# Kernel tuning notes

Hardware: AMD Instinct MI355X
Metric: run time of the kernel (lower is better)

Reference implementation:

```python
import jax, jax.numpy as jnp
import numpy as np

EMIN = 1e-9
EMAX = 1.0
PENAL = 3.0
VOLFRAC = 0.4
GAMMA2 = 1.0
NME = 262144        # number of finite elements
KE = 64             # 8x8 element stiffness entries per element
NDOF = 524288       # global degrees of freedom


def setup_inputs() -> dict:
    key = jax.random.key(0)
    k1, k2, k3, k4, k5 = jax.random.split(key, 5)
    W_x = jax.random.normal(k1, (NME,), dtype=jnp.float32)
    K_sep = jax.random.normal(k2, (NME, KE), dtype=jnp.float32)
    indeces_K = jax.random.randint(k3, (2, NME * KE), 0, NDOF, dtype=jnp.int32)
    u = jax.random.normal(k4, (NDOF,), dtype=jnp.float32)
    f = jax.random.normal(k5, (NDOF,), dtype=jnp.float32)
    return {"W_x": W_x, "K_sep": K_sep, "indeces_K": indeces_K, "u": u, "f": f}


def reference(W_x, K_sep, indeces_K, u, f):
    # SIMP density from logits
    rho = jax.nn.sigmoid(W_x)                                  # [nme]
    # power-law material interpolation: Emin + rho^p (Emax - Emin)
    scale = EMIN + rho ** PENAL * (EMAX - EMIN)                # [nme]
    # scaled element stiffness values, flattened COO values
    sK = (K_sep * scale[:, None]).reshape(-1)                  # [nme*64]
    rows = indeces_K[0]
    cols = indeces_K[1]
    # sparse matvec K @ u via gather + segment-sum scatter assembly
    Ku = jax.ops.segment_sum(sK * u[cols], rows, num_segments=NDOF)  # [ndof]
    confidence_loss = jnp.linalg.norm(Ku - f)
    vofrac_loss = jax.nn.relu(rho.mean() - VOLFRAC)
    loss = vofrac_loss + GAMMA2 * confidence_loss
    return loss
```

## Files before the change

kernel.cpp:

```cpp
#include <hip/hip_runtime.h>
#include <math.h>

namespace {

constexpr int       kNME    = 262144;
constexpr int       kNDOF   = 524288;
constexpr long long kNNZ    = 16777216;
constexpr int       kNB     = 64;
constexpr int       kBShift = 13;
constexpr int       kBSpan  = 8192;
constexpr int       kEnt    = 2048;
constexpr int       kPerTh  = 8;
constexpr int       kCtrStride = 16;

constexpr float kEmin    = 1e-9f;
constexpr float kEmax    = 1.0f;
constexpr float kVolfrac = 0.4f;

using u32   = unsigned;
using i32x4 = __attribute__((ext_vector_type(4))) int;
using f32x4 = __attribute__((ext_vector_type(4))) float;
using u32x4 = __attribute__((ext_vector_type(4))) unsigned;

__device__ __forceinline__ u32 pack32(unsigned localrow, float v) {
    return (localrow << 19) | (__float_as_uint(v) >> 13);
}

__global__ void scale_kernel(const float* __restrict__ W_x,
                             float* __restrict__ scale,
                             float* __restrict__ rho_sum) {
    int i = blockIdx.x * blockDim.x + threadIdx.x;
    float rho = 0.0f;
    if (i < kNME) {
        float x = W_x[i];
        rho = 1.0f / (1.0f + __expf(-x));
        scale[i] = kEmin + rho * rho * rho * (kEmax - kEmin);
    }
    for (int off = 32; off > 0; off >>= 1) rho += __shfl_down(rho, off, 64);
    __shared__ float partial[4];
    const int lane = threadIdx.x & 63;
    const int wid  = threadIdx.x >> 6;
    if (lane == 0) partial[wid] = rho;
    __syncthreads();
    if (threadIdx.x == 0)
        atomicAdd(rho_sum, partial[0] + partial[1] + partial[2] + partial[3]);
}

__global__ __launch_bounds__(256, 8)
void producer_kernel(const float* __restrict__ K_sep,
                     const int*   __restrict__ rows,
                     const int*   __restrict__ cols,
                     const float* __restrict__ u,
                     const float* __restrict__ scale,
                     u32*         __restrict__ pairs,
                     unsigned*    __restrict__ counters,
                     long long chunk_base, unsigned capSub, int R) {
    __shared__ unsigned hist[kNB], ofs[kNB], gbase[kNB];
    __shared__ u32      sorted[kEnt];

    const int tid = threadIdx.x;
    const int sub = blockIdx.x & (R - 1);
    if (tid < kNB) hist[tid] = 0u;
    __syncthreads();

    const long long i0 =
        chunk_base + (long long)blockIdx.x * kEnt + (long long)tid * kPerTh;
    i32x4 r0 = __builtin_nontemporal_load((const i32x4*)(rows + i0));
    i32x4 r1 = __builtin_nontemporal_load((const i32x4*)(rows + i0) + 1);
    i32x4 c0 = __builtin_nontemporal_load((const i32x4*)(cols + i0));
    i32x4 c1 = __builtin_nontemporal_load((const i32x4*)(cols + i0) + 1);
    f32x4 k0 = __builtin_nontemporal_load((const f32x4*)(K_sep + i0));
    f32x4 k1 = __builtin_nontemporal_load((const f32x4*)(K_sep + i0) + 1);
    const float s = scale[(int)(i0 >> 6)];

    unsigned rv[kPerTh];
    float    vv[kPerTh];
#pragma unroll
    for (int j = 0; j < 4; ++j) {
        rv[j]     = (unsigned)r0[j];  vv[j]     = k0[j] * s * u[c0[j]];
        rv[j + 4] = (unsigned)r1[j];  vv[j + 4] = k1[j] * s * u[c1[j]];
    }
#pragma unroll
    for (int j = 0; j < kPerTh; ++j)
        rv[j] |= atomicAdd(&hist[rv[j] >> kBShift], 1u) << 19;
    __syncthreads();

    if (tid < kNB) {
        unsigned h = hist[tid];
        unsigned x = h;
#pragma unroll
        for (int off = 1; off < kNB; off <<= 1) {
            unsigned y = __shfl_up(x, off, 64);
            if (tid >= off) x += y;
        }
        ofs[tid]   = x - h;
        gbase[tid] = atomicAdd(&counters[(tid * R + sub) * kCtrStride], h);
    }
    __syncthreads();

#pragma unroll
    for (int j = 0; j < kPerTh; ++j) {
        unsigned row = rv[j] & 0x7FFFFu;
        unsigned b   = row >> kBShift;
        unsigned pos = ofs[b] + (rv[j] >> 19);
        sorted[pos]  = pack32(row & (kBSpan - 1), vv[j]);
    }
    __syncthreads();

    const int wid = tid >> 6, lane = tid & 63;
    for (int b = wid; b < kNB; b += 4) {
        const unsigned s0 = ofs[b];
        const unsigned n  = hist[b];
        const unsigned g  = gbase[b];
        u32* dst = pairs + (size_t)(b * R + sub) * capSub + g;
        for (unsigned i = lane; i < n; i += 64) {
            if (g + i < capSub)
                __builtin_nontemporal_store(sorted[s0 + i], &dst[i]);
        }
    }
}

__global__ __launch_bounds__(512, 8)
void consumer_kernel(const u32*      __restrict__ pairs,
                     const unsigned* __restrict__ counters,
                     float*          __restrict__ partial,
                     unsigned capSub, int R, int accum) {
    const int b   = blockIdx.x / R;
    const int sub = blockIdx.x - b * R;
    unsigned cnt = counters[(b * R + sub) * kCtrStride];
    if (cnt > capSub) cnt = capSub;

    __shared__ float acc[kBSpan];
    for (int i = threadIdx.x; i < kBSpan; i += 512) acc[i] = 0.0f;
    __syncthreads();

    const u32* p = pairs + (size_t)(b * R + sub) * capSub;
    const unsigned aligned = cnt & ~3u;
    for (unsigned i = 4 * threadIdx.x; i < aligned; i += 4 * 512) {
        u32x4 e = __builtin_nontemporal_load((const u32x4*)(p + i));
#pragma unroll
        for (int j = 0; j < 4; ++j)
            atomicAdd(&acc[e[j] >> 19], __uint_as_float(e[j] << 13));
    }
    if (threadIdx.x < (cnt - aligned)) {
        u32 e = p[aligned + threadIdx.x];
        atomicAdd(&acc[e >> 19], __uint_as_float(e << 13));
    }
    __syncthreads();

    float* dst = partial + (size_t)(b * R + sub) * kBSpan;
    if (accum) {
        for (int i = threadIdx.x; i < kBSpan; i += 512) dst[i] += acc[i];
    } else {
        for (int i = threadIdx.x; i < kBSpan; i += 512) dst[i] = acc[i];
    }
}

__global__ void norm_kernel(const float* __restrict__ partial,
                            const float* __restrict__ f,
                            float* __restrict__ norm_sum, int R) {
    const int b     = blockIdx.x >> 3;
    const int i0    = (blockIdx.x & 7) * 1024 + threadIdx.x * 4;
    f32x4 s = {0.0f, 0.0f, 0.0f, 0.0f};
    for (int r = 0; r < R; ++r)
        s += *(const f32x4*)(partial + (size_t)(b * R + r) * kBSpan + i0);
    f32x4 fv = *(const f32x4*)(f + (size_t)b * kBSpan + i0);
    f32x4 d  = s - fv;
    float a = d[0] * d[0] + d[1] * d[1] + d[2] * d[2] + d[3] * d[3];
    for (int off = 32; off > 0; off >>= 1) a += __shfl_down(a, off, 64);
    __shared__ float partial_s[4];
    const int lane = threadIdx.x & 63;
    const int wid  = threadIdx.x >> 6;
    if (lane == 0) partial_s[wid] = a;
    __syncthreads();
    if (threadIdx.x == 0)
        atomicAdd(norm_sum,
                  partial_s[0] + partial_s[1] + partial_s[2] + partial_s[3]);
}

__global__ void scatter_dev_kernel(const float* __restrict__ K_sep,
                                   const int*   __restrict__ rows,
                                   const int*   __restrict__ cols,
                                   const float* __restrict__ u,
                                   const float* __restrict__ scale,
                                   float* __restrict__ Ku) {
    long long i = (long long)blockIdx.x * blockDim.x + threadIdx.x;
    if (i >= kNNZ) return;
    float s = scale[(int)(i >> 6)];
    atomicAdd(&Ku[rows[i]], K_sep[i] * s * u[cols[i]]);
}

__global__ void norm1_kernel(const float* __restrict__ Ku,
                             const float* __restrict__ f,
                             float* __restrict__ norm_sum) {
    float a = 0.0f;
    for (int i = blockIdx.x * blockDim.x + threadIdx.x; i < kNDOF;
         i += gridDim.x * blockDim.x) {
        float d = Ku[i] - f[i];
        a += d * d;
    }
    for (int off = 32; off > 0; off >>= 1) a += __shfl_down(a, off, 64);
    __shared__ float partial_s[4];
    const int lane = threadIdx.x & 63;
    const int wid  = threadIdx.x >> 6;
    if (lane == 0) partial_s[wid] = a;
    __syncthreads();
    if (threadIdx.x == 0)
        atomicAdd(norm_sum,
                  partial_s[0] + partial_s[1] + partial_s[2] + partial_s[3]);
}

__global__ void finalize_kernel(const float* __restrict__ acc,
                                float* __restrict__ out) {
    if (threadIdx.x == 0 && blockIdx.x == 0) {
        float rho_mean = acc[0] * (1.0f / (float)kNME);
        float vol = fmaxf(rho_mean - kVolfrac, 0.0f);
        out[0] = vol + sqrtf(acc[1]);
    }
}

}

extern "C" void kernel_launch(void* const* d_in, const int* in_sizes, int n_in,
                              void* d_out, int out_size, void* d_ws, size_t ws_size,
                              hipStream_t stream) {
    const float* W_x   = (const float*)d_in[0];
    const float* K_sep = (const float*)d_in[1];
    const int*   idx   = (const int*)d_in[2];
    const float* u     = (const float*)d_in[3];
    const float* f     = (const float*)d_in[4];
    const int* rows = idx;
    const int* cols = idx + kNNZ;

    float* ws = (float*)d_ws;
    const size_t avail = ws_size / sizeof(float);

    struct Opt { int nc, R; unsigned margin; };
    const Opt opts[] = {{1, 16, 2048}, {1, 16, 1024}, {1, 8, 2048},
                        {2, 8, 2048},  {2, 8, 1024},  {4, 8, 1024},
                        {4, 4, 1024},  {8, 4, 1024}};
    int NC = -1, R = 16;
    unsigned capSub = 0;
    size_t ctrF = 0, partialF = 0;
    for (const Opt& o : opts) {
        long long perCell = kNNZ / ((long long)o.nc * kNB * o.R);
        unsigned  mc      = (unsigned)perCell + o.margin;
        size_t cf = (size_t)o.nc * kNB * o.R * kCtrStride;
        size_t pf = (size_t)kNB * o.R * kBSpan;
        size_t need = 16 + cf + pf + (size_t)kNME +
                      (size_t)kNB * o.R * (size_t)mc;
        if (need <= avail) {
            NC = o.nc; R = o.R; capSub = mc; ctrF = cf; partialF = pf;
            break;
        }
    }

    if (NC < 0) {
        float* Ku    = ws;
        float* scale = ws + kNDOF;
        float* acc   = ws + kNDOF + kNME;
        hipMemsetAsync(ws, 0, (size_t)(kNDOF + kNME + 16) * sizeof(float), stream);
        scale_kernel<<<kNME / 256, 256, 0, stream>>>(W_x, scale, acc);
        scatter_dev_kernel<<<(int)(kNNZ / 256), 256, 0, stream>>>(
            K_sep, rows, cols, u, scale, Ku);
        norm1_kernel<<<2048, 256, 0, stream>>>(Ku, f, acc + 1);
        finalize_kernel<<<1, 64, 0, stream>>>(acc, (float*)d_out);
        return;
    }

    float*    acc      = ws;
    unsigned* counters = (unsigned*)(ws + 16);
    float*    partial  = ws + 16 + ctrF;
    float*    scale    = partial + partialF;
    u32*      pairs    = (u32*)(scale + kNME);

    hipMemsetAsync(ws, 0, (16 + ctrF) * sizeof(float), stream);

    scale_kernel<<<kNME / 256, 256, 0, stream>>>(W_x, scale, acc);

    const long long chunk = kNNZ / NC;
    const int prod_blocks = (int)(chunk / kEnt);
    for (int c = 0; c < NC; ++c) {
        unsigned* ctr = counters + (size_t)c * kNB * R * kCtrStride;
        producer_kernel<<<prod_blocks, 256, 0, stream>>>(
            K_sep, rows, cols, u, scale, pairs, ctr, chunk * c, capSub, R);
        consumer_kernel<<<kNB * R, 512, 0, stream>>>(
            pairs, ctr, partial, capSub, R, c > 0 ? 1 : 0);
    }

    norm_kernel<<<kNB * (kBSpan / 1024), 256, 0, stream>>>(
        partial, f, acc + 1, R);

    finalize_kernel<<<1, 64, 0, stream>>>(acc, (float*)d_out);
}
```

Measured before the change: 258.9 us.

## Double producer work per block and vectorize padded bucket writes

```diff
diff --git a/kernel.cpp b/kernel.cpp
--- a/kernel.cpp
+++ b/kernel.cpp
@@ -9,8 +9,9 @@
 constexpr int       kNB     = 64;
 constexpr int       kBShift = 13;
 constexpr int       kBSpan  = 8192;
-constexpr int       kEnt    = 2048;
-constexpr int       kPerTh  = 8;
+constexpr int       kEnt    = 4096;
+constexpr int       kPerTh  = 16;
+constexpr int       kSortN  = kEnt + kNB * 4;
 constexpr int       kCtrStride = 16;
 
 constexpr float kEmin    = 1e-9f;
@@ -46,7 +47,7 @@
         atomicAdd(rho_sum, partial[0] + partial[1] + partial[2] + partial[3]);
 }
 
-__global__ __launch_bounds__(256, 8)
+__global__ __launch_bounds__(256, 6)
 void producer_kernel(const float* __restrict__ K_sep,
                      const int*   __restrict__ rows,
                      const int*   __restrict__ cols,
@@ -55,46 +56,69 @@
                      u32*         __restrict__ pairs,
                      unsigned*    __restrict__ counters,
                      long long chunk_base, unsigned capSub, int R) {
-    __shared__ unsigned hist[kNB], ofs[kNB], gbase[kNB];
-    __shared__ u32      sorted[kEnt];
+    __shared__ unsigned hist[kNB], ofs[kNB], gbase[kNB], h4s[kNB];
+    __shared__ __align__(16) u32 sorted[kSortN];
 
     const int tid = threadIdx.x;
     const int sub = blockIdx.x & (R - 1);
     if (tid < kNB) hist[tid] = 0u;
+    for (int i = tid; i < kSortN / 4; i += 256)
+        ((u32x4*)sorted)[i] = u32x4{0u, 0u, 0u, 0u};
     __syncthreads();
 
     const long long i0 =
         chunk_base + (long long)blockIdx.x * kEnt + (long long)tid * kPerTh;
-    i32x4 r0 = __builtin_nontemporal_load((const i32x4*)(rows + i0));
-    i32x4 r1 = __builtin_nontemporal_load((const i32x4*)(rows + i0) + 1);
-    i32x4 c0 = __builtin_nontemporal_load((const i32x4*)(cols + i0));
-    i32x4 c1 = __builtin_nontemporal_load((const i32x4*)(cols + i0) + 1);
-    f32x4 k0 = __builtin_nontemporal_load((const f32x4*)(K_sep + i0));
-    f32x4 k1 = __builtin_nontemporal_load((const f32x4*)(K_sep + i0) + 1);
     const float s = scale[(int)(i0 >> 6)];
 
     unsigned rv[kPerTh];
     float    vv[kPerTh];
-#pragma unroll
-    for (int j = 0; j < 4; ++j) {
-        rv[j]     = (unsigned)r0[j];  vv[j]     = k0[j] * s * u[c0[j]];
-        rv[j + 4] = (unsigned)r1[j];  vv[j + 4] = k1[j] * s * u[c1[j]];
-    }
-#pragma unroll
-    for (int j = 0; j < kPerTh; ++j)
-        rv[j] |= atomicAdd(&hist[rv[j] >> kBShift], 1u) << 19;
+    {
+        i32x4 r0 = __builtin_nontemporal_load((const i32x4*)(rows + i0));
+        i32x4 r1 = __builtin_nontemporal_load((const i32x4*)(rows + i0) + 1);
+        i32x4 c0 = __builtin_nontemporal_load((const i32x4*)(cols + i0));
+        i32x4 c1 = __builtin_nontemporal_load((const i32x4*)(cols + i0) + 1);
+        f32x4 k0 = __builtin_nontemporal_load((const f32x4*)(K_sep + i0));
+        f32x4 k1 = __builtin_nontemporal_load((const f32x4*)(K_sep + i0) + 1);
+#pragma unroll
+        for (int j = 0; j < 4; ++j) {
+            rv[j]     = (unsigned)r0[j];  vv[j]     = k0[j] * s * u[c0[j]];
+            rv[j + 4] = (unsigned)r1[j];  vv[j + 4] = k1[j] * s * u[c1[j]];
+        }
+#pragma unroll
+        for (int j = 0; j < 8; ++j)
+            rv[j] |= atomicAdd(&hist[rv[j] >> kBShift], 1u) << 19;
+    }
+    {
+        const long long i8 = i0 + 8;
+        i32x4 r0 = __builtin_nontemporal_load((const i32x4*)(rows + i8));
+        i32x4 r1 = __builtin_nontemporal_load((const i32x4*)(rows + i8) + 1);
+        i32x4 c0 = __builtin_nontemporal_load((const i32x4*)(cols + i8));
+        i32x4 c1 = __builtin_nontemporal_load((const i32x4*)(cols + i8) + 1);
+        f32x4 k0 = __builtin_nontemporal_load((const f32x4*)(K_sep + i8));
+        f32x4 k1 = __builtin_nontemporal_load((const f32x4*)(K_sep + i8) + 1);
+#pragma unroll
+        for (int j = 0; j < 4; ++j) {
+            rv[8 + j]  = (unsigned)r0[j];  vv[8 + j]  = k0[j] * s * u[c0[j]];
+            rv[12 + j] = (unsigned)r1[j];  vv[12 + j] = k1[j] * s * u[c1[j]];
+        }
+#pragma unroll
+        for (int j = 8; j < 16; ++j)
+            rv[j] |= atomicAdd(&hist[rv[j] >> kBShift], 1u) << 19;
+    }
     __syncthreads();
 
     if (tid < kNB) {
-        unsigned h = hist[tid];
-        unsigned x = h;
+        unsigned h  = hist[tid];
+        unsigned h4 = (h + 3u) & ~3u;
+        unsigned x  = h4;
 #pragma unroll
         for (int off = 1; off < kNB; off <<= 1) {
             unsigned y = __shfl_up(x, off, 64);
             if (tid >= off) x += y;
         }
-        ofs[tid]   = x - h;
-        gbase[tid] = atomicAdd(&counters[(tid * R + sub) * kCtrStride], h);
+        ofs[tid]   = x - h4;
+        h4s[tid]   = h4;
+        gbase[tid] = atomicAdd(&counters[(tid * R + sub) * kCtrStride], h4);
     }
     __syncthreads();
 
@@ -110,12 +134,14 @@
     const int wid = tid >> 6, lane = tid & 63;
     for (int b = wid; b < kNB; b += 4) {
         const unsigned s0 = ofs[b];
-        const unsigned n  = hist[b];
+        const unsigned n4 = h4s[b];
         const unsigned g  = gbase[b];
+        if (g >= capSub) continue;
+        const unsigned m = min(n4, capSub - g);
         u32* dst = pairs + (size_t)(b * R + sub) * capSub + g;
-        for (unsigned i = lane; i < n; i += 64) {
-            if (g + i < capSub)
-                __builtin_nontemporal_store(sorted[s0 + i], &dst[i]);
+        for (unsigned i = lane * 4; i < m; i += 256) {
+            u32x4 w = *(const u32x4*)&sorted[s0 + i];
+            __builtin_nontemporal_store(w, (u32x4*)(dst + i));
         }
     }
 }
@@ -159,8 +185,8 @@
 __global__ void norm_kernel(const float* __restrict__ partial,
                             const float* __restrict__ f,
                             float* __restrict__ norm_sum, int R) {
-    const int b     = blockIdx.x >> 3;
-    const int i0    = (blockIdx.x & 7) * 1024 + threadIdx.x * 4;
+    const int b  = blockIdx.x >> 3;
+    const int i0 = (blockIdx.x & 7) * 1024 + threadIdx.x * 4;
     f32x4 s = {0.0f, 0.0f, 0.0f, 0.0f};
     for (int r = 0; r < R; ++r)
         s += *(const f32x4*)(partial + (size_t)(b * R + r) * kBSpan + i0);
```

New measurement: 281.0 us. 8.5% more time.

## Fuse scale and finalize into producer/norm, pad buckets for vector stores

Applied to the files above, without the earlier changes.

```diff
diff --git a/kernel.cpp b/kernel.cpp
--- a/kernel.cpp
+++ b/kernel.cpp
@@ -11,6 +11,7 @@
 constexpr int       kBSpan  = 8192;
 constexpr int       kEnt    = 2048;
 constexpr int       kPerTh  = 8;
+constexpr int       kSortN  = kEnt + kNB * 4;
 constexpr int       kCtrStride = 16;
 
 constexpr float kEmin    = 1e-9f;
@@ -24,26 +25,6 @@
 
 __device__ __forceinline__ u32 pack32(unsigned localrow, float v) {
     return (localrow << 19) | (__float_as_uint(v) >> 13);
-}
-
-__global__ void scale_kernel(const float* __restrict__ W_x,
-                             float* __restrict__ scale,
-                             float* __restrict__ rho_sum) {
-    int i = blockIdx.x * blockDim.x + threadIdx.x;
-    float rho = 0.0f;
-    if (i < kNME) {
-        float x = W_x[i];
-        rho = 1.0f / (1.0f + __expf(-x));
-        scale[i] = kEmin + rho * rho * rho * (kEmax - kEmin);
-    }
-    for (int off = 32; off > 0; off >>= 1) rho += __shfl_down(rho, off, 64);
-    __shared__ float partial[4];
-    const int lane = threadIdx.x & 63;
-    const int wid  = threadIdx.x >> 6;
-    if (lane == 0) partial[wid] = rho;
-    __syncthreads();
-    if (threadIdx.x == 0)
-        atomicAdd(rho_sum, partial[0] + partial[1] + partial[2] + partial[3]);
 }
 
 __global__ __launch_bounds__(256, 8)
@@ -51,27 +32,35 @@
                      const int*   __restrict__ rows,
                      const int*   __restrict__ cols,
                      const float* __restrict__ u,
-                     const float* __restrict__ scale,
+                     const float* __restrict__ W_x,
                      u32*         __restrict__ pairs,
                      unsigned*    __restrict__ counters,
+                     float*       __restrict__ rho_sum,
                      long long chunk_base, unsigned capSub, int R) {
     __shared__ unsigned hist[kNB], ofs[kNB], gbase[kNB];
-    __shared__ u32      sorted[kEnt];
+    __shared__ __align__(16) u32 sorted[kSortN];
+    __shared__ float rho_part[4];
 
     const int tid = threadIdx.x;
     const int sub = blockIdx.x & (R - 1);
     if (tid < kNB) hist[tid] = 0u;
+    for (int i = tid; i < kSortN / 4; i += 256)
+        ((u32x4*)sorted)[i] = u32x4{0u, 0u, 0u, 0u};
     __syncthreads();
 
     const long long i0 =
         chunk_base + (long long)blockIdx.x * kEnt + (long long)tid * kPerTh;
+
+    const float x   = W_x[(int)(i0 >> 6)];
+    const float rho = 1.0f / (1.0f + __expf(-x));
+    const float s   = kEmin + rho * rho * rho * (kEmax - kEmin);
+
     i32x4 r0 = __builtin_nontemporal_load((const i32x4*)(rows + i0));
     i32x4 r1 = __builtin_nontemporal_load((const i32x4*)(rows + i0) + 1);
     i32x4 c0 = __builtin_nontemporal_load((const i32x4*)(cols + i0));
     i32x4 c1 = __builtin_nontemporal_load((const i32x4*)(cols + i0) + 1);
     f32x4 k0 = __builtin_nontemporal_load((const f32x4*)(K_sep + i0));
     f32x4 k1 = __builtin_nontemporal_load((const f32x4*)(K_sep + i0) + 1);
-    const float s = scale[(int)(i0 >> 6)];
 
     unsigned rv[kPerTh];
     float    vv[kPerTh];
@@ -83,18 +72,27 @@
 #pragma unroll
     for (int j = 0; j < kPerTh; ++j)
         rv[j] |= atomicAdd(&hist[rv[j] >> kBShift], 1u) << 19;
-    __syncthreads();
+
+    {
+        float rt = ((tid & 7) == 0) ? rho : 0.0f;
+        for (int off = 32; off > 0; off >>= 1) rt += __shfl_down(rt, off, 64);
+        if ((tid & 63) == 0) rho_part[tid >> 6] = rt;
+    }
+    __syncthreads();
+    if (tid == 0)
+        atomicAdd(rho_sum,
+                  rho_part[0] + rho_part[1] + rho_part[2] + rho_part[3]);
 
     if (tid < kNB) {
-        unsigned h = hist[tid];
-        unsigned x = h;
+        unsigned h4 = (hist[tid] + 3u) & ~3u;
+        unsigned x4 = h4;
 #pragma unroll
         for (int off = 1; off < kNB; off <<= 1) {
-            unsigned y = __shfl_up(x, off, 64);
-            if (tid >= off) x += y;
-        }
-        ofs[tid]   = x - h;
-        gbase[tid] = atomicAdd(&counters[(tid * R + sub) * kCtrStride], h);
+            unsigned y = __shfl_up(x4, off, 64);
+            if (tid >= off) x4 += y;
+        }
+        ofs[tid]   = x4 - h4;
+        gbase[tid] = atomicAdd(&counters[(tid * R + sub) * kCtrStride], h4);
     }
     __syncthreads();
 
@@ -110,12 +108,14 @@
     const int wid = tid >> 6, lane = tid & 63;
     for (int b = wid; b < kNB; b += 4) {
         const unsigned s0 = ofs[b];
-        const unsigned n  = hist[b];
+        const unsigned n4 = (hist[b] + 3u) & ~3u;
         const unsigned g  = gbase[b];
+        if (g >= capSub) continue;
+        const unsigned m = min(n4, capSub - g);
         u32* dst = pairs + (size_t)(b * R + sub) * capSub + g;
-        for (unsigned i = lane; i < n; i += 64) {
-            if (g + i < capSub)
-                __builtin_nontemporal_store(sorted[s0 + i], &dst[i]);
+        for (unsigned i = lane * 4; i < m; i += 256) {
+            u32x4 w = *(const u32x4*)&sorted[s0 + i];
+            __builtin_nontemporal_store(w, (u32x4*)(dst + i));
         }
     }
 }
@@ -135,32 +135,36 @@
     __syncthreads();
 
     const u32* p = pairs + (size_t)(b * R + sub) * capSub;
-    const unsigned aligned = cnt & ~3u;
-    for (unsigned i = 4 * threadIdx.x; i < aligned; i += 4 * 512) {
+    unsigned i = 4 * threadIdx.x;
+    if (i < cnt) {
         u32x4 e = __builtin_nontemporal_load((const u32x4*)(p + i));
+        for (i += 2048; i < cnt; i += 2048) {
+            u32x4 n = __builtin_nontemporal_load((const u32x4*)(p + i));
+#pragma unroll
+            for (int j = 0; j < 4; ++j)
+                atomicAdd(&acc[e[j] >> 19], __uint_as_float(e[j] << 13));
+            e = n;
+        }
 #pragma unroll
         for (int j = 0; j < 4; ++j)
             atomicAdd(&acc[e[j] >> 19], __uint_as_float(e[j] << 13));
     }
-    if (threadIdx.x < (cnt - aligned)) {
-        u32 e = p[aligned + threadIdx.x];
-        atomicAdd(&acc[e >> 19], __uint_as_float(e << 13));
-    }
     __syncthreads();
 
     float* dst = partial + (size_t)(b * R + sub) * kBSpan;
     if (accum) {
-        for (int i = threadIdx.x; i < kBSpan; i += 512) dst[i] += acc[i];
+        for (int k = threadIdx.x; k < kBSpan; k += 512) dst[k] += acc[k];
     } else {
-        for (int i = threadIdx.x; i < kBSpan; i += 512) dst[i] = acc[i];
+        for (int k = threadIdx.x; k < kBSpan; k += 512) dst[k] = acc[k];
     }
 }
 
 __global__ void norm_kernel(const float* __restrict__ partial,
                             const float* __restrict__ f,
-                            float* __restrict__ norm_sum, int R) {
-    const int b     = blockIdx.x >> 3;
-    const int i0    = (blockIdx.x & 7) * 1024 + threadIdx.x * 4;
+                            float* __restrict__ acc,
+                            float* __restrict__ out, int R) {
+    const int b  = blockIdx.x >> 3;
+    const int i0 = (blockIdx.x & 7) * 1024 + threadIdx.x * 4;
     f32x4 s = {0.0f, 0.0f, 0.0f, 0.0f};
     for (int r = 0; r < R; ++r)
         s += *(const f32x4*)(partial + (size_t)(b * R + r) * kBSpan + i0);
@@ -173,9 +177,40 @@
     const int wid  = threadIdx.x >> 6;
     if (lane == 0) partial_s[wid] = a;
     __syncthreads();
+    if (threadIdx.x == 0) {
+        atomicAdd(&acc[1],
+                  partial_s[0] + partial_s[1] + partial_s[2] + partial_s[3]);
+        __threadfence();
+        unsigned done = atomicAdd((unsigned*)&acc[2], 1u);
+        if (done == gridDim.x - 1) {
+            float rs = __hip_atomic_load(&acc[0], __ATOMIC_RELAXED,
+                                         __HIP_MEMORY_SCOPE_AGENT);
+            float ns = __hip_atomic_load(&acc[1], __ATOMIC_RELAXED,
+                                         __HIP_MEMORY_SCOPE_AGENT);
+            float rho_mean = rs * (1.0f / (float)kNME);
+            out[0] = fmaxf(rho_mean - kVolfrac, 0.0f) + sqrtf(ns);
+        }
+    }
+}
+
+__global__ void scale_kernel(const float* __restrict__ W_x,
+                             float* __restrict__ scale,
+                             float* __restrict__ rho_sum) {
+    int i = blockIdx.x * blockDim.x + threadIdx.x;
+    float rho = 0.0f;
+    if (i < kNME) {
+        float x = W_x[i];
+        rho = 1.0f / (1.0f + __expf(-x));
+        scale[i] = kEmin + rho * rho * rho * (kEmax - kEmin);
+    }
+    for (int off = 32; off > 0; off >>= 1) rho += __shfl_down(rho, off, 64);
+    __shared__ float partial[4];
+    const int lane = threadIdx.x & 63;
+    const int wid  = threadIdx.x >> 6;
+    if (lane == 0) partial[wid] = rho;
+    __syncthreads();
     if (threadIdx.x == 0)
-        atomicAdd(norm_sum,
-                  partial_s[0] + partial_s[1] + partial_s[2] + partial_s[3]);
+        atomicAdd(rho_sum, partial[0] + partial[1] + partial[2] + partial[3]);
 }
 
 __global__ void scatter_dev_kernel(const float* __restrict__ K_sep,
@@ -247,8 +282,7 @@
         unsigned  mc      = (unsigned)perCell + o.margin;
         size_t cf = (size_t)o.nc * kNB * o.R * kCtrStride;
         size_t pf = (size_t)kNB * o.R * kBSpan;
-        size_t need = 16 + cf + pf + (size_t)kNME +
-                      (size_t)kNB * o.R * (size_t)mc;
+        size_t need = 16 + cf + pf + (size_t)kNB * o.R * (size_t)mc;
         if (need <= avail) {
             NC = o.nc; R = o.R; capSub = mc; ctrF = cf; partialF = pf;
             break;
@@ -271,25 +305,20 @@
     float*    acc      = ws;
     unsigned* counters = (unsigned*)(ws + 16);
     float*    partial  = ws + 16 + ctrF;
-    float*    scale    = partial + partialF;
-    u32*      pairs    = (u32*)(scale + kNME);
+    u32*      pairs    = (u32*)(partial + partialF);
 
     hipMemsetAsync(ws, 0, (16 + ctrF) * sizeof(float), stream);
-
-    scale_kernel<<<kNME / 256, 256, 0, stream>>>(W_x, scale, acc);
 
     const long long chunk = kNNZ / NC;
     const int prod_blocks = (int)(chunk / kEnt);
     for (int c = 0; c < NC; ++c) {
         unsigned* ctr = counters + (size_t)c * kNB * R * kCtrStride;
         producer_kernel<<<prod_blocks, 256, 0, stream>>>(
-            K_sep, rows, cols, u, scale, pairs, ctr, chunk * c, capSub, R);
+            K_sep, rows, cols, u, W_x, pairs, ctr, acc, chunk * c, capSub, R);
         consumer_kernel<<<kNB * R, 512, 0, stream>>>(
             pairs, ctr, partial, capSub, R, c > 0 ? 1 : 0);
     }
 
     norm_kernel<<<kNB * (kBSpan / 1024), 256, 0, stream>>>(
-        partial, f, acc + 1, R);
-
-    finalize_kernel<<<1, 64, 0, stream>>>(acc, (float*)d_out);
-}
+        partial, f, acc, (float*)d_out, R);
+}
```

After: 270.3 us. +4.4%, slower.

## Fuse consumer, norm and finalize into one per-bucket kernel for single-chunk path

Applied to the files above, without the earlier changes.

```diff
diff --git a/kernel.cpp b/kernel.cpp
--- a/kernel.cpp
+++ b/kernel.cpp
@@ -120,6 +120,67 @@
     }
 }
 
+__global__ __launch_bounds__(1024, 4)
+void consumer_norm_kernel(const u32*      __restrict__ pairs,
+                          const unsigned* __restrict__ counters,
+                          const float*    __restrict__ f,
+                          float*          __restrict__ acc_g,
+                          float*          __restrict__ out,
+                          unsigned capSub, int R) {
+    const int b = blockIdx.x;
+    __shared__ float tile[kBSpan];
+    __shared__ float wpart[16];
+    for (int i = threadIdx.x; i < kBSpan / 4; i += 1024)
+        ((f32x4*)tile)[i] = f32x4{0.0f, 0.0f, 0.0f, 0.0f};
+    __syncthreads();
+
+    for (int sub = 0; sub < R; ++sub) {
+        unsigned cnt = counters[(b * R + sub) * kCtrStride];
+        if (cnt > capSub) cnt = capSub;
+        const u32* p = pairs + (size_t)(b * R + sub) * capSub;
+        const unsigned aligned = cnt & ~3u;
+        for (unsigned i = 4 * threadIdx.x; i < aligned; i += 4096) {
+            u32x4 e = __builtin_nontemporal_load((const u32x4*)(p + i));
+#pragma unroll
+            for (int j = 0; j < 4; ++j)
+                atomicAdd(&tile[e[j] >> 19], __uint_as_float(e[j] << 13));
+        }
+        if (threadIdx.x < (cnt - aligned)) {
+            u32 e = p[aligned + threadIdx.x];
+            atomicAdd(&tile[e >> 19], __uint_as_float(e << 13));
+        }
+    }
+    __syncthreads();
+
+    float a = 0.0f;
+    for (int k = 4 * threadIdx.x; k < kBSpan; k += 4096) {
+        f32x4 t  = *(const f32x4*)&tile[k];
+        f32x4 fv = *(const f32x4*)(f + (size_t)b * kBSpan + k);
+        f32x4 d  = t - fv;
+        a += d[0] * d[0] + d[1] * d[1] + d[2] * d[2] + d[3] * d[3];
+    }
+    for (int off = 32; off > 0; off >>= 1) a += __shfl_down(a, off, 64);
+    const int lane = threadIdx.x & 63, wid = threadIdx.x >> 6;
+    if (lane == 0) wpart[wid] = a;
+    __syncthreads();
+    if (threadIdx.x == 0) {
+        float t = 0.0f;
+#pragma unroll
+        for (int w = 0; w < 16; ++w) t += wpart[w];
+        atomicAdd(&acc_g[1], t);
+        __threadfence();
+        unsigned done = atomicAdd((unsigned*)&acc_g[2], 1u);
+        if (done == gridDim.x - 1) {
+            float rs = __hip_atomic_load(&acc_g[0], __ATOMIC_RELAXED,
+                                         __HIP_MEMORY_SCOPE_AGENT);
+            float ns = __hip_atomic_load(&acc_g[1], __ATOMIC_RELAXED,
+                                         __HIP_MEMORY_SCOPE_AGENT);
+            float rho_mean = rs * (1.0f / (float)kNME);
+            out[0] = fmaxf(rho_mean - kVolfrac, 0.0f) + sqrtf(ns);
+        }
+    }
+}
+
 __global__ __launch_bounds__(512, 8)
 void consumer_kernel(const u32*      __restrict__ pairs,
                      const unsigned* __restrict__ counters,
@@ -136,7 +197,7 @@
 
     const u32* p = pairs + (size_t)(b * R + sub) * capSub;
     const unsigned aligned = cnt & ~3u;
-    for (unsigned i = 4 * threadIdx.x; i < aligned; i += 4 * 512) {
+    for (unsigned i = 4 * threadIdx.x; i < aligned; i += 2048) {
         u32x4 e = __builtin_nontemporal_load((const u32x4*)(p + i));
 #pragma unroll
         for (int j = 0; j < 4; ++j)
@@ -150,17 +211,18 @@
 
     float* dst = partial + (size_t)(b * R + sub) * kBSpan;
     if (accum) {
-        for (int i = threadIdx.x; i < kBSpan; i += 512) dst[i] += acc[i];
+        for (int k = threadIdx.x; k < kBSpan; k += 512) dst[k] += acc[k];
     } else {
-        for (int i = threadIdx.x; i < kBSpan; i += 512) dst[i] = acc[i];
+        for (int k = threadIdx.x; k < kBSpan; k += 512) dst[k] = acc[k];
     }
 }
 
 __global__ void norm_kernel(const float* __restrict__ partial,
                             const float* __restrict__ f,
-                            float* __restrict__ norm_sum, int R) {
-    const int b     = blockIdx.x >> 3;
-    const int i0    = (blockIdx.x & 7) * 1024 + threadIdx.x * 4;
+                            float* __restrict__ acc,
+                            float* __restrict__ out, int R) {
+    const int b  = blockIdx.x >> 3;
+    const int i0 = (blockIdx.x & 7) * 1024 + threadIdx.x * 4;
     f32x4 s = {0.0f, 0.0f, 0.0f, 0.0f};
     for (int r = 0; r < R; ++r)
         s += *(const f32x4*)(partial + (size_t)(b * R + r) * kBSpan + i0);
@@ -173,9 +235,20 @@
     const int wid  = threadIdx.x >> 6;
     if (lane == 0) partial_s[wid] = a;
     __syncthreads();
-    if (threadIdx.x == 0)
-        atomicAdd(norm_sum,
+    if (threadIdx.x == 0) {
+        atomicAdd(&acc[1],
                   partial_s[0] + partial_s[1] + partial_s[2] + partial_s[3]);
+        __threadfence();
+        unsigned done = atomicAdd((unsigned*)&acc[2], 1u);
+        if (done == gridDim.x - 1) {
+            float rs = __hip_atomic_load(&acc[0], __ATOMIC_RELAXED,
+                                         __HIP_MEMORY_SCOPE_AGENT);
+            float ns = __hip_atomic_load(&acc[1], __ATOMIC_RELAXED,
+                                         __HIP_MEMORY_SCOPE_AGENT);
+            float rho_mean = rs * (1.0f / (float)kNME);
+            out[0] = fmaxf(rho_mean - kVolfrac, 0.0f) + sqrtf(ns);
+        }
+    }
 }
 
 __global__ void scatter_dev_kernel(const float* __restrict__ K_sep,
@@ -246,7 +319,7 @@
         long long perCell = kNNZ / ((long long)o.nc * kNB * o.R);
         unsigned  mc      = (unsigned)perCell + o.margin;
         size_t cf = (size_t)o.nc * kNB * o.R * kCtrStride;
-        size_t pf = (size_t)kNB * o.R * kBSpan;
+        size_t pf = (o.nc > 1) ? (size_t)kNB * o.R * kBSpan : 0;
         size_t need = 16 + cf + pf + (size_t)kNME +
                       (size_t)kNB * o.R * (size_t)mc;
         if (need <= avail) {
@@ -280,16 +353,20 @@
 
     const long long chunk = kNNZ / NC;
     const int prod_blocks = (int)(chunk / kEnt);
-    for (int c = 0; c < NC; ++c) {
-        unsigned* ctr = counters + (size_t)c * kNB * R * kCtrStride;
+    if (NC == 1) {
         producer_kernel<<<prod_blocks, 256, 0, stream>>>(
-            K_sep, rows, cols, u, scale, pairs, ctr, chunk * c, capSub, R);
-        consumer_kernel<<<kNB * R, 512, 0, stream>>>(
-            pairs, ctr, partial, capSub, R, c > 0 ? 1 : 0);
-    }
-
-    norm_kernel<<<kNB * (kBSpan / 1024), 256, 0, stream>>>(
-        partial, f, acc + 1, R);
-
-    finalize_kernel<<<1, 64, 0, stream>>>(acc, (float*)d_out);
-}
+            K_sep, rows, cols, u, scale, pairs, counters, 0LL, capSub, R);
+        consumer_norm_kernel<<<kNB, 1024, 0, stream>>>(
+            pairs, counters, f, acc, (float*)d_out, capSub, R);
+    } else {
+        for (int c = 0; c < NC; ++c) {
+            unsigned* ctr = counters + (size_t)c * kNB * R * kCtrStride;
+            producer_kernel<<<prod_blocks, 256, 0, stream>>>(
+                K_sep, rows, cols, u, scale, pairs, ctr, chunk * c, capSub, R);
+            consumer_kernel<<<kNB * R, 512, 0, stream>>>(
+                pairs, ctr, partial, capSub, R, c > 0 ? 1 : 0);
+        }
+        norm_kernel<<<kNB * (kBSpan / 1024), 256, 0, stream>>>(
+            partial, f, acc, (float*)d_out, R);
+    }
+}
```

Result: slower. 489.3 us (+89.0%).
